# Optimization experiments

Hardware: AMD Instinct MI355X
Metric: run time of the kernel (lower is better)

## Reference

```python
import jax, jax.numpy as jnp
import numpy as np

EVENTLEN = 8  # config.event_length
NEG = -10000.0


def setup_inputs() -> dict:
    key = jax.random.key(0)
    k1, k2 = jax.random.split(key)
    T, B, E = 128, 512, 128  # decodelen, batch_size, entity_size
    feats = jax.random.normal(k1, (T, B, E), dtype=jnp.float32)
    transitions = jax.random.normal(k2, (E, E), dtype=jnp.float32)
    # Same masking the torch module applies to transitions.data at init
    transitions = transitions.at[0, :].set(NEG).at[:, -1].set(NEG)
    return {"feats": feats, "transitions": transitions}


def reference(feats, transitions):
    """Segmented CRF forward algorithm (OneCrfCCKSDecoder._forward_alg).

    feats:       [T, B, E] per-step emission scores (entity tag logits)
    transitions: [E, E]    transitions[j, k] = score of k -> j
    Returns scalar alpha / (T // EVENTLEN).
    """
    T, B, E = feats.shape
    n_events = T // EVENTLEN

    # Faithful to torch: init_alphas[:][0] = 0.0 zeroes the batch-0 ROW.
    init_fv = jnp.full((B, E), NEG, dtype=feats.dtype).at[0].set(0.0)

    t_idx = jnp.arange(T)
    is_boundary = (t_idx % EVENTLEN == 0) & (t_idx != 0)  # accumulate alpha
    is_update = (t_idx % EVENTLEN != 0)                   # DP update step

    def step(carry, inp):
        fv, alpha = carry              # fv: [B, E], alpha: scalar
        feat, bnd, upd = inp           # feat: [B, E]
        # Event-boundary accumulation (uses fv BEFORE any update; note the
        # original never resets fv inside _forward_alg).
        alpha_inc = jnp.mean(jax.nn.logsumexp(fv + transitions[-1], axis=1))
        alpha = alpha + jnp.where(bnd, alpha_inc, jnp.zeros_like(alpha_inc))
        # fv_new[b, j] = logsumexp_k( fv[b,k] + feat[b,k] + transitions[j,k] )
        x = fv + feat                                        # [B, E]
        fv_new = jax.nn.logsumexp(x[:, None, :] + transitions[None, :, :], axis=-1)
        fv = jnp.where(upd, fv_new, fv)
        return (fv, alpha), None

    (fv, alpha), _ = jax.lax.scan(
        step, (init_fv, jnp.zeros((), feats.dtype)), (feats, is_boundary, is_update)
    )
    # Terminal accumulation after the loop.
    alpha = alpha + jnp.mean(jax.nn.logsumexp(fv + transitions[-1], axis=1))
    return alpha / n_events
```

## Files before the change

### kernel.cpp

```cpp
#include <hip/hip_runtime.h>


typedef _Float16 f16x4 __attribute__((ext_vector_type(4)));
typedef _Float16 f16x8 __attribute__((ext_vector_type(8)));
typedef float    f32x4 __attribute__((ext_vector_type(4)));

#define NEG_VAL   (-10000.0f)
#define C_SCALE   0.0024787521766663585f
#define LOG_C     6.0f

#define LDS_BARRIER() asm volatile("s_waitcnt lgkmcnt(0)\n\ts_barrier" ::: "memory")

__global__ __launch_bounds__(512)
void crf_fwd(const float* __restrict__ feats,
             const float* __restrict__ trans,
             float* __restrict__ out)
{
    const int tid  = threadIdx.x;
    const int w    = tid >> 6;
    const int lane = tid & 63;
    const int bloc = lane & 15;
    const int q    = lane >> 4;
    const int b    = blockIdx.x * 16 + bloc;

    f16x8 Afrag[4];
    {
        const float* rowp = trans + (size_t)(16 * w + bloc) * 128;
        #pragma unroll
        for (int kap = 0; kap < 4; ++kap) {
            const f32x4* p = (const f32x4*)(rowp + 32 * kap + 8 * q);
            f32x4 x = p[0], y = p[1];
            f16x8 f;
            f[0] = (_Float16)__expf(x[0]); f[1] = (_Float16)__expf(x[1]);
            f[2] = (_Float16)__expf(x[2]); f[3] = (_Float16)__expf(x[3]);
            f[4] = (_Float16)__expf(y[0]); f[5] = (_Float16)__expf(y[1]);
            f[6] = (_Float16)__expf(y[2]); f[7] = (_Float16)__expf(y[3]);
            Afrag[kap] = f;
        }
    }
    f32x4 te;
    {
        f32x4 x = *(const f32x4*)(trans + 127 * 128 + 16 * w + 4 * q);
        te[0] = __expf(x[0]); te[1] = __expf(x[1]);
        te[2] = __expf(x[2]); te[3] = __expf(x[3]);
    }

    __shared__ __align__(16) char  Hbuf[4096];
    __shared__ float Spart[16 * 8];
    __shared__ float Mpart[16 * 8];

    const int waddr = bloc * 256 + (((2 * w + (q >> 1)) ^ bloc) * 16) + 8 * (q & 1);
    int raddr[4];
    #pragma unroll
    for (int kap = 0; kap < 4; ++kap)
        raddr[kap] = bloc * 256 + (((4 * kap + q) ^ bloc) * 16);

    const float* fb = feats + (size_t)b * 128 + 16 * w + 4 * q;
    f32x4 efi;
    f32x4 r1v, r2v;
    {
        f32x4 x = *(const f32x4*)(fb + 1 * 65536);
        efi[0] = __expf(x[0]) * C_SCALE; efi[1] = __expf(x[1]) * C_SCALE;
        efi[2] = __expf(x[2]) * C_SCALE; efi[3] = __expf(x[3]) * C_SCALE;
        r1v = *(const f32x4*)(fb + 2 * 65536);
        r2v = *(const f32x4*)(fb + 3 * 65536);
    }
    float logc_cur = LOG_C;

    f32x4 acc = {1.f, 1.f, 1.f, 1.f};
    float M     = (b == 0) ? 0.0f : NEG_VAL;
    float alpha = 0.0f;

    #pragma unroll 8
    for (int t = 1; t < 128; ++t) {
        const bool upd = (t & 7) != 0;
        float sc_next = C_SCALE;
        float lg_next = LOG_C;

        if (upd) {
            M += logc_cur;
            f16x4 hh;
            hh[0] = (_Float16)(acc[0] * efi[0]);
            hh[1] = (_Float16)(acc[1] * efi[1]);
            hh[2] = (_Float16)(acc[2] * efi[2]);
            hh[3] = (_Float16)(acc[3] * efi[3]);
            *(f16x4*)(Hbuf + waddr) = hh;
            LDS_BARRIER();

            f16x8 B0 = *(const f16x8*)(Hbuf + raddr[0]);
            f16x8 B1 = *(const f16x8*)(Hbuf + raddr[1]);
            f16x8 B2 = *(const f16x8*)(Hbuf + raddr[2]);
            f16x8 B3 = *(const f16x8*)(Hbuf + raddr[3]);

            f32x4 z = {0.f, 0.f, 0.f, 0.f};
            f32x4 da = __builtin_amdgcn_mfma_f32_16x16x32_f16(Afrag[0], B0, z, 0, 0, 0);
            f32x4 db = __builtin_amdgcn_mfma_f32_16x16x32_f16(Afrag[1], B1, z, 0, 0, 0);
            da = __builtin_amdgcn_mfma_f32_16x16x32_f16(Afrag[2], B2, da, 0, 0, 0);
            db = __builtin_amdgcn_mfma_f32_16x16x32_f16(Afrag[3], B3, db, 0, 0, 0);
            acc = da + db;
        } else {
            float s = acc[0] * te[0] + acc[1] * te[1]
                    + acc[2] * te[2] + acc[3] * te[3];
            float m = fmaxf(fmaxf(acc[0], acc[1]), fmaxf(acc[2], acc[3]));
            s += __shfl_xor(s, 16, 64);
            s += __shfl_xor(s, 32, 64);
            m = fmaxf(m, __shfl_xor(m, 16, 64));
            m = fmaxf(m, __shfl_xor(m, 32, 64));
            if (q == 0) {
                Spart[bloc * 8 + w] = s;
                Mpart[bloc * 8 + w] = m;
            }
            LDS_BARRIER();

            f32x4 sa = *(const f32x4*)&Spart[bloc * 8];
            f32x4 sb = *(const f32x4*)&Spart[bloc * 8 + 4];
            f32x4 ma = *(const f32x4*)&Mpart[bloc * 8];
            f32x4 mb = *(const f32x4*)&Mpart[bloc * 8 + 4];
            float r = ((sa[0] + sa[1]) + (sa[2] + sa[3]))
                    + ((sb[0] + sb[1]) + (sb[2] + sb[3]));
            float cmax = fmaxf(fmaxf(fmaxf(ma[0], ma[1]), fmaxf(ma[2], ma[3])),
                               fmaxf(fmaxf(mb[0], mb[1]), fmaxf(mb[2], mb[3])));

            alpha += M + __logf(r);
            sc_next = C_SCALE * __builtin_amdgcn_rcpf(cmax);
            lg_next = LOG_C + __logf(cmax);
        }

        if (t + 1 < 128) {
            efi[0] = __expf(r1v[0]) * sc_next; efi[1] = __expf(r1v[1]) * sc_next;
            efi[2] = __expf(r1v[2]) * sc_next; efi[3] = __expf(r1v[3]) * sc_next;
            logc_cur = lg_next;
            r1v = r2v;
            if (t + 3 < 128) r2v = *(const f32x4*)(fb + (size_t)(t + 3) * 65536);
        }
    }

    {
        float s = acc[0] * te[0] + acc[1] * te[1]
                + acc[2] * te[2] + acc[3] * te[3];
        s += __shfl_xor(s, 16, 64);
        s += __shfl_xor(s, 32, 64);
        if (q == 0) Spart[bloc * 8 + w] = s;
        LDS_BARRIER();
        f32x4 sa = *(const f32x4*)&Spart[bloc * 8];
        f32x4 sb = *(const f32x4*)&Spart[bloc * 8 + 4];
        float r = ((sa[0] + sa[1]) + (sa[2] + sa[3]))
                + ((sb[0] + sb[1]) + (sb[2] + sb[3]));
        alpha += M + __logf(r);
    }

    if (w == 0) {
        float v = alpha;
        #pragma unroll
        for (int off = 1; off < 64; off <<= 1)
            v += __shfl_xor(v, off, 64);
        if (lane == 0)
            atomicAdd(out, v * (1.0f / (4.0f * 512.0f * 16.0f)));
    }
}

extern "C" void kernel_launch(void* const* d_in, const int* in_sizes, int n_in,
                              void* d_out, int out_size, void* d_ws, size_t ws_size,
                              hipStream_t stream) {
    const float* feats = (const float*)d_in[0];
    const float* trans = (const float*)d_in[1];
    float* out = (float*)d_out;

    hipMemsetAsync(out, 0, sizeof(float), stream);
    crf_fwd<<<32, 512, 0, stream>>>(feats, trans, out);
}
```

Baseline: 114.0 us.

## Collapse eight-wave block into a single wave per batch tile

Each block now uses one 64-lane wave that computes all eight output tiles itself, holding the full transition fragments, feature prefetches and accumulators in registers. This removes the block-wide LDS barriers and the cross-wave partial-sum and max exchange through shared memory at each step. The cost is that each lane does eight times the MFMA, exp and conversion work serially per step, and register pressure rises sharply. With only 32 blocks, the step latency now depends on single-wave throughput rather than barrier cost.

```diff
diff --git a/kernel.cpp b/kernel.cpp
--- a/kernel.cpp
+++ b/kernel.cpp
@@ -9,23 +9,20 @@
 #define C_SCALE   0.0024787521766663585f
 #define LOG_C     6.0f
 
-#define LDS_BARRIER() asm volatile("s_waitcnt lgkmcnt(0)\n\ts_barrier" ::: "memory")
-
-__global__ __launch_bounds__(512)
+__global__ __launch_bounds__(64, 1)
 void crf_fwd(const float* __restrict__ feats,
              const float* __restrict__ trans,
              float* __restrict__ out)
 {
-    const int tid  = threadIdx.x;
-    const int w    = tid >> 6;
-    const int lane = tid & 63;
+    const int lane = threadIdx.x & 63;
     const int bloc = lane & 15;
     const int q    = lane >> 4;
     const int b    = blockIdx.x * 16 + bloc;
 
-    f16x8 Afrag[4];
-    {
-        const float* rowp = trans + (size_t)(16 * w + bloc) * 128;
+    f16x8 Afrag[8][4];
+    #pragma unroll
+    for (int jt = 0; jt < 8; ++jt) {
+        const float* rowp = trans + (size_t)(16 * jt + bloc) * 128;
         #pragma unroll
         for (int kap = 0; kap < 4; ++kap) {
             const f32x4* p = (const f32x4*)(rowp + 32 * kap + 8 * q);
@@ -35,39 +32,42 @@
             f[2] = (_Float16)__expf(x[2]); f[3] = (_Float16)__expf(x[3]);
             f[4] = (_Float16)__expf(y[0]); f[5] = (_Float16)__expf(y[1]);
             f[6] = (_Float16)__expf(y[2]); f[7] = (_Float16)__expf(y[3]);
-            Afrag[kap] = f;
+            Afrag[jt][kap] = f;
         }
     }
-    f32x4 te;
-    {
-        f32x4 x = *(const f32x4*)(trans + 127 * 128 + 16 * w + 4 * q);
-        te[0] = __expf(x[0]); te[1] = __expf(x[1]);
-        te[2] = __expf(x[2]); te[3] = __expf(x[3]);
+    f32x4 te[8];
+    #pragma unroll
+    for (int jt = 0; jt < 8; ++jt) {
+        f32x4 x = *(const f32x4*)(trans + 127 * 128 + 16 * jt + 4 * q);
+        te[jt][0] = __expf(x[0]); te[jt][1] = __expf(x[1]);
+        te[jt][2] = __expf(x[2]); te[jt][3] = __expf(x[3]);
     }
 
-    __shared__ __align__(16) char  Hbuf[4096];
-    __shared__ float Spart[16 * 8];
-    __shared__ float Mpart[16 * 8];
+    __shared__ __align__(16) char Hbuf[4096];
 
-    const int waddr = bloc * 256 + (((2 * w + (q >> 1)) ^ bloc) * 16) + 8 * (q & 1);
-    int raddr[4];
+    int waddr[8], raddr[4];
+    #pragma unroll
+    for (int jt = 0; jt < 8; ++jt)
+        waddr[jt] = bloc * 256 + (((2 * jt + (q >> 1)) ^ bloc) * 16) + 8 * (q & 1);
     #pragma unroll
     for (int kap = 0; kap < 4; ++kap)
         raddr[kap] = bloc * 256 + (((4 * kap + q) ^ bloc) * 16);
 
-    const float* fb = feats + (size_t)b * 128 + 16 * w + 4 * q;
-    f32x4 efi;
-    f32x4 r1v, r2v;
-    {
-        f32x4 x = *(const f32x4*)(fb + 1 * 65536);
-        efi[0] = __expf(x[0]) * C_SCALE; efi[1] = __expf(x[1]) * C_SCALE;
-        efi[2] = __expf(x[2]) * C_SCALE; efi[3] = __expf(x[3]) * C_SCALE;
-        r1v = *(const f32x4*)(fb + 2 * 65536);
-        r2v = *(const f32x4*)(fb + 3 * 65536);
+    const float* fb = feats + (size_t)b * 128 + 4 * q;
+    f32x4 efi[8], r1v[8], r2v[8];
+    #pragma unroll
+    for (int jt = 0; jt < 8; ++jt) {
+        f32x4 x = *(const f32x4*)(fb + 1 * 65536 + 16 * jt);
+        efi[jt][0] = __expf(x[0]) * C_SCALE; efi[jt][1] = __expf(x[1]) * C_SCALE;
+        efi[jt][2] = __expf(x[2]) * C_SCALE; efi[jt][3] = __expf(x[3]) * C_SCALE;
+        r1v[jt] = *(const f32x4*)(fb + 2 * 65536 + 16 * jt);
+        r2v[jt] = *(const f32x4*)(fb + 3 * 65536 + 16 * jt);
     }
     float logc_cur = LOG_C;
 
-    f32x4 acc = {1.f, 1.f, 1.f, 1.f};
+    f32x4 acc[8];
+    #pragma unroll
+    for (int jt = 0; jt < 8; ++jt) acc[jt] = (f32x4){1.f, 1.f, 1.f, 1.f};
     float M     = (b == 0) ? 0.0f : NEG_VAL;
     float alpha = 0.0f;
 
@@ -79,84 +79,87 @@
 
         if (upd) {
             M += logc_cur;
-            f16x4 hh;
-            hh[0] = (_Float16)(acc[0] * efi[0]);
-            hh[1] = (_Float16)(acc[1] * efi[1]);
-            hh[2] = (_Float16)(acc[2] * efi[2]);
-            hh[3] = (_Float16)(acc[3] * efi[3]);
-            *(f16x4*)(Hbuf + waddr) = hh;
-            LDS_BARRIER();
-
+            __builtin_amdgcn_wave_barrier();
+            #pragma unroll
+            for (int jt = 0; jt < 8; ++jt) {
+                f16x4 hh;
+                hh[0] = (_Float16)(acc[jt][0] * efi[jt][0]);
+                hh[1] = (_Float16)(acc[jt][1] * efi[jt][1]);
+                hh[2] = (_Float16)(acc[jt][2] * efi[jt][2]);
+                hh[3] = (_Float16)(acc[jt][3] * efi[jt][3]);
+                *(f16x4*)(Hbuf + waddr[jt]) = hh;
+            }
+            __builtin_amdgcn_wave_barrier();
             f16x8 B0 = *(const f16x8*)(Hbuf + raddr[0]);
             f16x8 B1 = *(const f16x8*)(Hbuf + raddr[1]);
             f16x8 B2 = *(const f16x8*)(Hbuf + raddr[2]);
             f16x8 B3 = *(const f16x8*)(Hbuf + raddr[3]);
 
             f32x4 z = {0.f, 0.f, 0.f, 0.f};
-            f32x4 da = __builtin_amdgcn_mfma_f32_16x16x32_f16(Afrag[0], B0, z, 0, 0, 0);
-            f32x4 db = __builtin_amdgcn_mfma_f32_16x16x32_f16(Afrag[1], B1, z, 0, 0, 0);
-            da = __builtin_amdgcn_mfma_f32_16x16x32_f16(Afrag[2], B2, da, 0, 0, 0);
-            db = __builtin_amdgcn_mfma_f32_16x16x32_f16(Afrag[3], B3, db, 0, 0, 0);
-            acc = da + db;
+            #pragma unroll
+            for (int jt = 0; jt < 8; ++jt) {
+                f32x4 da = __builtin_amdgcn_mfma_f32_16x16x32_f16(Afrag[jt][0], B0, z, 0, 0, 0);
+                f32x4 db = __builtin_amdgcn_mfma_f32_16x16x32_f16(Afrag[jt][1], B1, z, 0, 0, 0);
+                da = __builtin_amdgcn_mfma_f32_16x16x32_f16(Afrag[jt][2], B2, da, 0, 0, 0);
+                db = __builtin_amdgcn_mfma_f32_16x16x32_f16(Afrag[jt][3], B3, db, 0, 0, 0);
+                acc[jt] = da + db;
+            }
         } else {
-            float s = acc[0] * te[0] + acc[1] * te[1]
-                    + acc[2] * te[2] + acc[3] * te[3];
-            float m = fmaxf(fmaxf(acc[0], acc[1]), fmaxf(acc[2], acc[3]));
+            float sp[8];
+            float m = acc[0][0];
+            #pragma unroll
+            for (int jt = 0; jt < 8; ++jt) {
+                sp[jt] = acc[jt][0] * te[jt][0] + acc[jt][1] * te[jt][1]
+                       + acc[jt][2] * te[jt][2] + acc[jt][3] * te[jt][3];
+                m = fmaxf(m, fmaxf(fmaxf(acc[jt][0], acc[jt][1]),
+                                   fmaxf(acc[jt][2], acc[jt][3])));
+            }
+            float s = ((sp[0] + sp[1]) + (sp[2] + sp[3]))
+                    + ((sp[4] + sp[5]) + (sp[6] + sp[7]));
             s += __shfl_xor(s, 16, 64);
             s += __shfl_xor(s, 32, 64);
             m = fmaxf(m, __shfl_xor(m, 16, 64));
             m = fmaxf(m, __shfl_xor(m, 32, 64));
-            if (q == 0) {
-                Spart[bloc * 8 + w] = s;
-                Mpart[bloc * 8 + w] = m;
-            }
-            LDS_BARRIER();
 
-            f32x4 sa = *(const f32x4*)&Spart[bloc * 8];
-            f32x4 sb = *(const f32x4*)&Spart[bloc * 8 + 4];
-            f32x4 ma = *(const f32x4*)&Mpart[bloc * 8];
-            f32x4 mb = *(const f32x4*)&Mpart[bloc * 8 + 4];
-            float r = ((sa[0] + sa[1]) + (sa[2] + sa[3]))
-                    + ((sb[0] + sb[1]) + (sb[2] + sb[3]));
-            float cmax = fmaxf(fmaxf(fmaxf(ma[0], ma[1]), fmaxf(ma[2], ma[3])),
-                               fmaxf(fmaxf(mb[0], mb[1]), fmaxf(mb[2], mb[3])));
-
-            alpha += M + __logf(r);
-            sc_next = C_SCALE * __builtin_amdgcn_rcpf(cmax);
-            lg_next = LOG_C + __logf(cmax);
+            alpha += M + __logf(s);
+            sc_next = C_SCALE * __builtin_amdgcn_rcpf(m);
+            lg_next = LOG_C + __logf(m);
         }
 
         if (t + 1 < 128) {
-            efi[0] = __expf(r1v[0]) * sc_next; efi[1] = __expf(r1v[1]) * sc_next;
-            efi[2] = __expf(r1v[2]) * sc_next; efi[3] = __expf(r1v[3]) * sc_next;
+            #pragma unroll
+            for (int jt = 0; jt < 8; ++jt) {
+                efi[jt][0] = __expf(r1v[jt][0]) * sc_next;
+                efi[jt][1] = __expf(r1v[jt][1]) * sc_next;
+                efi[jt][2] = __expf(r1v[jt][2]) * sc_next;
+                efi[jt][3] = __expf(r1v[jt][3]) * sc_next;
+                r1v[jt] = r2v[jt];
+                if (t + 3 < 128)
+                    r2v[jt] = *(const f32x4*)(fb + (size_t)(t + 3) * 65536 + 16 * jt);
+            }
             logc_cur = lg_next;
-            r1v = r2v;
-            if (t + 3 < 128) r2v = *(const f32x4*)(fb + (size_t)(t + 3) * 65536);
         }
     }
 
     {
-        float s = acc[0] * te[0] + acc[1] * te[1]
-                + acc[2] * te[2] + acc[3] * te[3];
+        float sp[8];
+        #pragma unroll
+        for (int jt = 0; jt < 8; ++jt)
+            sp[jt] = acc[jt][0] * te[jt][0] + acc[jt][1] * te[jt][1]
+                   + acc[jt][2] * te[jt][2] + acc[jt][3] * te[jt][3];
+        float s = ((sp[0] + sp[1]) + (sp[2] + sp[3]))
+                + ((sp[4] + sp[5]) + (sp[6] + sp[7]));
         s += __shfl_xor(s, 16, 64);
         s += __shfl_xor(s, 32, 64);
-        if (q == 0) Spart[bloc * 8 + w] = s;
-        LDS_BARRIER();
-        f32x4 sa = *(const f32x4*)&Spart[bloc * 8];
-        f32x4 sb = *(const f32x4*)&Spart[bloc * 8 + 4];
-        float r = ((sa[0] + sa[1]) + (sa[2] + sa[3]))
-                + ((sb[0] + sb[1]) + (sb[2] + sb[3]));
-        alpha += M + __logf(r);
+        alpha += M + __logf(s);
     }
 
-    if (w == 0) {
-        float v = alpha;
-        #pragma unroll
-        for (int off = 1; off < 64; off <<= 1)
-            v += __shfl_xor(v, off, 64);
-        if (lane == 0)
-            atomicAdd(out, v * (1.0f / (4.0f * 512.0f * 16.0f)));
-    }
+    float v = alpha;
+    #pragma unroll
+    for (int off = 1; off < 64; off <<= 1)
+        v += __shfl_xor(v, off, 64);
+    if (lane == 0)
+        atomicAdd(out, v * (1.0f / (4.0f * 512.0f * 16.0f)));
 }
 
 extern "C" void kernel_launch(void* const* d_in, const int* in_sizes, int n_in,
@@ -167,5 +170,5 @@
     float* out = (float*)d_out;
 
     hipMemsetAsync(out, 0, sizeof(float), stream);
-    crf_fwd<<<32, 512, 0, stream>>>(feats, trans, out);
+    crf_fwd<<<32, 64, 0, stream>>>(feats, trans, out);
 }
```

Measured after the change: 200.6 us. +76.0%, slower.

## Precompute scaled exp of emissions in separate fp16 kernel and double-buffer LDS

Applied to the files above, without the earlier changes.

Adds a fully parallel pre-pass kernel that computes exp(feats)*scale, converts it to fp16 and writes it to workspace in a layout matched to the serial kernel's per-lane reads. The serial CRF recurrence then loads half-size fp16 values and multiplies in fp16, with no exps on its critical path. The LDS exchange buffer is double-buffered so the next step's writes cannot race with the previous step's reads. Renormalisation at boundaries now rescales the accumulator directly instead of folding into the next emission scale. The cost is an extra kernel launch, a workspace write/read pass, and lower fp16 precision in the product.

```diff
diff --git a/kernel.cpp b/kernel.cpp
--- a/kernel.cpp
+++ b/kernel.cpp
@@ -11,8 +11,41 @@
 
 #define LDS_BARRIER() asm volatile("s_waitcnt lgkmcnt(0)\n\ts_barrier" ::: "memory")
 
+__global__ __launch_bounds__(256)
+void prep_exp(const float* __restrict__ feats, _Float16* __restrict__ ef)
+{
+    int id = blockIdx.x * 256 + threadIdx.x;
+    #pragma unroll
+    for (int it = 0; it < 4; ++it, id += 524288) {
+        const int jj = id & 31;
+        const int tb = id >> 5;
+        const int b  = tb & 511;
+        const int t  = tb >> 9;
+        f32x4 x = *(const f32x4*)(feats + (size_t)tb * 128 + 4 * jj);
+        auto lo = __builtin_amdgcn_cvt_pkrtz(__expf(x[0]) * C_SCALE,
+                                             __expf(x[1]) * C_SCALE);
+        auto hi = __builtin_amdgcn_cvt_pkrtz(__expf(x[2]) * C_SCALE,
+                                             __expf(x[3]) * C_SCALE);
+        f16x4 o;
+        o[0] = (_Float16)lo[0]; o[1] = (_Float16)lo[1];
+        o[2] = (_Float16)hi[0]; o[3] = (_Float16)hi[1];
+        const int off = t * 65536 + (b >> 4) * 2048 + (jj >> 2) * 256
+                      + (b & 15) * 16 + (jj & 3) * 4;
+        *(f16x4*)(ef + off) = o;
+    }
+}
+
+__device__ inline f16x4 cvt4(f32x4 a) {
+    auto lo = __builtin_amdgcn_cvt_pkrtz(a[0], a[1]);
+    auto hi = __builtin_amdgcn_cvt_pkrtz(a[2], a[3]);
+    f16x4 o;
+    o[0] = (_Float16)lo[0]; o[1] = (_Float16)lo[1];
+    o[2] = (_Float16)hi[0]; o[3] = (_Float16)hi[1];
+    return o;
+}
+
 __global__ __launch_bounds__(512)
-void crf_fwd(const float* __restrict__ feats,
+void crf_fwd(const _Float16* __restrict__ ef,
              const float* __restrict__ trans,
              float* __restrict__ out)
 {
@@ -45,7 +78,7 @@
         te[2] = __expf(x[2]); te[3] = __expf(x[3]);
     }
 
-    __shared__ __align__(16) char  Hbuf[4096];
+    __shared__ __align__(16) char  Hbuf[8192];
     __shared__ float Spart[16 * 8];
     __shared__ float Mpart[16 * 8];
 
@@ -55,42 +88,31 @@
     for (int kap = 0; kap < 4; ++kap)
         raddr[kap] = bloc * 256 + (((4 * kap + q) ^ bloc) * 16);
 
-    const float* fb = feats + (size_t)b * 128 + 16 * w + 4 * q;
-    f32x4 efi;
-    f32x4 r1v, r2v;
-    {
-        f32x4 x = *(const f32x4*)(fb + 1 * 65536);
-        efi[0] = __expf(x[0]) * C_SCALE; efi[1] = __expf(x[1]) * C_SCALE;
-        efi[2] = __expf(x[2]) * C_SCALE; efi[3] = __expf(x[3]) * C_SCALE;
-        r1v = *(const f32x4*)(fb + 2 * 65536);
-        r2v = *(const f32x4*)(fb + 3 * 65536);
-    }
-    float logc_cur = LOG_C;
+    const _Float16* efb = ef + blockIdx.x * 2048 + w * 256 + bloc * 16 + q * 4;
+    f16x4 cur, nx1, nx2;
+    cur = *(const f16x4*)(efb + 1 * 65536);
+    nx1 = *(const f16x4*)(efb + 2 * 65536);
+    nx2 = *(const f16x4*)(efb + 3 * 65536);
 
     f32x4 acc = {1.f, 1.f, 1.f, 1.f};
     float M     = (b == 0) ? 0.0f : NEG_VAL;
     float alpha = 0.0f;
+    int hb = 0;
 
     #pragma unroll 8
     for (int t = 1; t < 128; ++t) {
         const bool upd = (t & 7) != 0;
-        float sc_next = C_SCALE;
-        float lg_next = LOG_C;
 
         if (upd) {
-            M += logc_cur;
-            f16x4 hh;
-            hh[0] = (_Float16)(acc[0] * efi[0]);
-            hh[1] = (_Float16)(acc[1] * efi[1]);
-            hh[2] = (_Float16)(acc[2] * efi[2]);
-            hh[3] = (_Float16)(acc[3] * efi[3]);
-            *(f16x4*)(Hbuf + waddr) = hh;
+            M += LOG_C;
+            f16x4 hh = cvt4(acc) * cur;
+            *(f16x4*)(Hbuf + hb + waddr) = hh;
             LDS_BARRIER();
 
-            f16x8 B0 = *(const f16x8*)(Hbuf + raddr[0]);
-            f16x8 B1 = *(const f16x8*)(Hbuf + raddr[1]);
-            f16x8 B2 = *(const f16x8*)(Hbuf + raddr[2]);
-            f16x8 B3 = *(const f16x8*)(Hbuf + raddr[3]);
+            f16x8 B0 = *(const f16x8*)(Hbuf + hb + raddr[0]);
+            f16x8 B1 = *(const f16x8*)(Hbuf + hb + raddr[1]);
+            f16x8 B2 = *(const f16x8*)(Hbuf + hb + raddr[2]);
+            f16x8 B3 = *(const f16x8*)(Hbuf + hb + raddr[3]);
 
             f32x4 z = {0.f, 0.f, 0.f, 0.f};
             f32x4 da = __builtin_amdgcn_mfma_f32_16x16x32_f16(Afrag[0], B0, z, 0, 0, 0);
@@ -98,6 +120,7 @@
             da = __builtin_amdgcn_mfma_f32_16x16x32_f16(Afrag[2], B2, da, 0, 0, 0);
             db = __builtin_amdgcn_mfma_f32_16x16x32_f16(Afrag[3], B3, db, 0, 0, 0);
             acc = da + db;
+            hb ^= 4096;
         } else {
             float s = acc[0] * te[0] + acc[1] * te[1]
                     + acc[2] * te[2] + acc[3] * te[3];
@@ -122,16 +145,15 @@
                                fmaxf(fmaxf(mb[0], mb[1]), fmaxf(mb[2], mb[3])));
 
             alpha += M + __logf(r);
-            sc_next = C_SCALE * __builtin_amdgcn_rcpf(cmax);
-            lg_next = LOG_C + __logf(cmax);
+            const float inv = __builtin_amdgcn_rcpf(cmax);
+            acc[0] *= inv; acc[1] *= inv; acc[2] *= inv; acc[3] *= inv;
+            M += __logf(cmax);
         }
 
         if (t + 1 < 128) {
-            efi[0] = __expf(r1v[0]) * sc_next; efi[1] = __expf(r1v[1]) * sc_next;
-            efi[2] = __expf(r1v[2]) * sc_next; efi[3] = __expf(r1v[3]) * sc_next;
-            logc_cur = lg_next;
-            r1v = r2v;
-            if (t + 3 < 128) r2v = *(const f32x4*)(fb + (size_t)(t + 3) * 65536);
+            cur = nx1;
+            nx1 = nx2;
+            if (t + 3 < 128) nx2 = *(const f16x4*)(efb + (size_t)(t + 3) * 65536);
         }
     }
 
@@ -165,7 +187,9 @@
     const float* feats = (const float*)d_in[0];
     const float* trans = (const float*)d_in[1];
     float* out = (float*)d_out;
+    _Float16* ef = (_Float16*)d_ws;
 
-    hipMemsetAsync(out, 0, sizeof(float), stream);
-    crf_fwd<<<32, 512, 0, stream>>>(feats, trans, out);
+    (void)hipMemsetAsync(out, 0, sizeof(float), stream);
+    prep_exp<<<2048, 256, 0, stream>>>(feats, ef);
+    crf_fwd<<<32, 512, 0, stream>>>(ef, trans, out);
 }
```

Result: faster. 106.2 us (-6.8%).
